# Optimization experiments

Hardware: AMD Instinct MI355X
Metric: run time of the kernel (lower is better)

Reference implementation:

```python
import jax, jax.numpy as jnp
import numpy as np

R = 10000   # relation_num
E = 256     # emb_size == hidden_size
B = 1024    # batch
L = 8       # body length (loop runs L-1 steps)


def setup_inputs() -> dict:
    key = jax.random.key(0)
    ks = jax.random.split(key, 10)
    s = 0.05
    return {
        "bodys": jax.random.randint(ks[0], (B, L), 0, R),
        "emb_w": jax.random.normal(ks[1], (R, E), jnp.float32) * s,
        "w_ih": jax.random.normal(ks[2], (4 * E, E), jnp.float32) * s,
        "w_hh": jax.random.normal(ks[3], (4 * E, E), jnp.float32) * s,
        "b_ih": jax.random.normal(ks[4], (4 * E,), jnp.float32) * s,
        "b_hh": jax.random.normal(ks[5], (4 * E,), jnp.float32) * s,
        "fc1_w": jax.random.normal(ks[6], (E, 2 * E), jnp.float32) * s,
        "fc1_b": jax.random.normal(ks[7], (E,), jnp.float32) * s,
        "fc2_w": jax.random.normal(ks[8], (R + 1, E), jnp.float32) * s,
        "fc2_b": jax.random.normal(ks[9], (R + 1,), jnp.float32) * s,
    }


def _lstm(x, w_ih, w_hh, b_ih, b_hh):
    # x: [B, L, E] -> hidden states [B, L, H] (torch gate order i,f,g,o)
    Bn, _, H = x.shape[0], x.shape[1], w_hh.shape[1]
    h0 = jnp.zeros((Bn, H), x.dtype)
    c0 = jnp.zeros((Bn, H), x.dtype)

    def step(carry, xt):
        h, c = carry
        g = xt @ w_ih.T + b_ih + h @ w_hh.T + b_hh
        i, f, gg, o = jnp.split(g, 4, axis=-1)
        c = jax.nn.sigmoid(f) * c + jax.nn.sigmoid(i) * jnp.tanh(gg)
        h = jax.nn.sigmoid(o) * jnp.tanh(c)
        return (h, c), h

    _, hs = jax.lax.scan(step, (h0, c0), x.transpose(1, 0, 2))
    return hs.transpose(1, 0, 2)


def reference(bodys, emb_w, w_ih, w_hh, b_ih, b_hh, fc1_w, fc1_b, fc2_w, fc2_b):
    x = emb_w[bodys]                       # [B, L, E] embedded body relations
    body_hid = _lstm(x, w_ih, w_hh, b_ih, b_hh)  # [B, L, E]
    Rn = emb_w.shape[0]
    prob = emb_concat = prob_sf = None
    for i in range(body_hid.shape[1] - 1):   # short fixed unroll (L-1 steps)
        if i == 0:
            emb_1 = x[:, 0, :]
            second = x[:, 1, :]
        else:
            # prob_sf @ cat(embedding(indices), body_hid[:, i])  without [B,R+1,E]
            emb_1 = prob_sf[:, :Rn] @ emb_w + prob_sf[:, Rn:] * body_hid[:, i, :]
            # relation_emb[:, i+1, :] == emb_w[i+1] broadcast over batch
            second = jnp.broadcast_to(emb_w[i + 1], emb_1.shape)
        emb_concat = jnp.concatenate([emb_1, second], axis=1)   # [B, 2E]
        prob = jax.nn.relu(emb_concat @ fc1_w.T + fc1_b) @ fc2_w.T + fc2_b  # [B, R+1]
        prob_sf = jax.nn.softmax(prob, axis=1)
    return prob, emb_concat
```

## Files before the change

### kernel.cpp

```cpp
#include <hip/hip_runtime.h>

#define Bv 1024
#define Ev 256
#define Lv 8
#define Rv 10000
#define NP1 10001
#define PS2 10240
#define NPAD 10112
#define BM 64
#define BN 128
#define NSLICE 16
#define NSLOT 158
#define RPSTRIDE 160

typedef __attribute__((ext_vector_type(8))) short bf16x8;
typedef __attribute__((ext_vector_type(4))) float f32x4;

__device__ __forceinline__ float b2f(unsigned short u) {
    union { unsigned int i; float f; } v; v.i = ((unsigned int)u) << 16; return v.f;
}
__device__ __forceinline__ unsigned short f2b(float f) {
    union { float f; unsigned int i; } v; v.f = f;
    unsigned int r = v.i + 0x7fffu + ((v.i >> 16) & 1u);
    return (unsigned short)(r >> 16);
}
__device__ __forceinline__ float ftanh(float x) {
    x = fminf(fmaxf(x, -30.f), 30.f);
    float e = __expf(2.f * x);
    return (e - 1.f) / (e + 1.f);
}
__device__ __forceinline__ void glds16(const void* g, void* l) {
    __builtin_amdgcn_global_load_lds(
        (const __attribute__((address_space(1))) void*)g,
        (__attribute__((address_space(3))) void*)l, 16, 0, 0);
}

__global__ __launch_bounds__(256) void gemm_tile(
    const unsigned short* __restrict__ A1, int lda1,
    const unsigned short* __restrict__ W1, int ldw1,
    const float* __restrict__ bias1,
    int Ktot, int kchunk, int Ncols, int mode,
    float* __restrict__ outF, unsigned short* __restrict__ outB, int ldc,
    float* __restrict__ rowPart, float* __restrict__ sfLastU)
{
    __shared__ unsigned short As[2][BM * 32];
    __shared__ unsigned short Bs[2][BN * 32];

    int bmode = mode & 7;
    int swz   = mode >> 4;
    int bx, by, bz;
    if (swz == 1) {
        int r = blockIdx.x & 7, q = blockIdx.x >> 3;
        bx = q & 15; by = r + (q >> 4) * 8; bz = 0;
        if (by >= NPAD / BN) return;
    } else if (swz == 2) {
        int r = blockIdx.x & 7, q = blockIdx.x >> 3;
        bz = r + (q >> 5) * 8; bx = (q & 31) >> 1; by = q & 1;
    } else {
        bx = blockIdx.x; by = blockIdx.y; bz = blockIdx.z;
    }

    int tid  = threadIdx.x;
    int wave = tid >> 6;
    int lane = tid & 63;
    int quad = lane >> 4;
    int l16  = lane & 15;
    int wm = (wave & 1) * 32;
    int wn = (wave >> 1) * 64;
    int m0 = bx * BM;
    int n0 = by * BN;
    int k0 = bz * kchunk;
    int k1 = k0 + kchunk; if (k1 > Ktot) k1 = Ktot;

    f32x4 acc[2][4];
#pragma unroll
    for (int i = 0; i < 2; ++i)
#pragma unroll
        for (int j = 0; j < 4; ++j) acc[i][j] = (f32x4){0.f, 0.f, 0.f, 0.f};

    int c0 = tid, c1 = 256 + tid;
    int row0 = c0 >> 2, row1 = c1 >> 2;
    int g80 = ((c0 & 3) ^ (row0 & 3) ^ ((row0 >> 2) & 3)) * 8;
    int g81 = ((c1 & 3) ^ (row1 & 3) ^ ((row1 >> 2) & 3)) * 8;

    bool first = true;
    for (int k = k0; k < k1; k += 64) {
        if (!first) __syncthreads();
        first = false;
#pragma unroll
        for (int h = 0; h < 2; ++h) {
            int kk = k + h * 32;
            glds16(A1 + (size_t)(m0 + row0) * lda1 + kk + g80, As[h] + (wave * 64) * 8);
            glds16(W1 + (size_t)(n0 + row0) * ldw1 + kk + g80, Bs[h] + (wave * 64) * 8);
            glds16(W1 + (size_t)(n0 + row1) * ldw1 + kk + g81, Bs[h] + (256 + wave * 64) * 8);
        }
        asm volatile("s_waitcnt vmcnt(0)" ::: "memory");
        __syncthreads();

#pragma unroll
        for (int h = 0; h < 2; ++h) {
            bf16x8 af[2], bfr[4];
#pragma unroll
            for (int t = 0; t < 2; ++t) {
                int m = wm + t * 16 + l16;
                int ca = quad ^ (m & 3) ^ ((m >> 2) & 3);
                af[t] = *(const bf16x8*)(As[h] + m * 32 + ca * 8);
            }
#pragma unroll
            for (int t = 0; t < 4; ++t) {
                int n = wn + t * 16 + l16;
                int cb = quad ^ (n & 3) ^ ((n >> 2) & 3);
                bfr[t] = *(const bf16x8*)(Bs[h] + n * 32 + cb * 8);
            }
#pragma unroll
            for (int i = 0; i < 2; ++i)
#pragma unroll
                for (int j = 0; j < 4; ++j)
                    acc[i][j] = __builtin_amdgcn_mfma_f32_16x16x32_bf16(
                        af[i], bfr[j], acc[i][j], 0, 0, 0);
        }
    }

    if (bmode == 5) {
        float rsum[2][4];
#pragma unroll
        for (int i = 0; i < 2; ++i)
#pragma unroll
            for (int r = 0; r < 4; ++r) rsum[i][r] = 0.f;
#pragma unroll
        for (int j = 0; j < 4; ++j) {
            int n = n0 + wn + j * 16 + l16;
            bool valid = (n < Ncols);
            float bsum = valid ? bias1[n] : 0.f;
#pragma unroll
            for (int i = 0; i < 2; ++i) {
                int mBase = m0 + wm + i * 16 + quad * 4;
#pragma unroll
                for (int r = 0; r < 4; ++r) {
                    float e = 0.f;
                    unsigned short w = 0;
                    if (valid) {
                        e = __expf(acc[i][j][r] + bsum);
                        w = f2b(e);
                        if (n == Rv) sfLastU[mBase + r] = e;
                    }
                    outB[(size_t)(mBase + r) * ldc + n] = w;
                    rsum[i][r] += e;
                }
            }
        }
        int slot = by * 2 + (wn >> 6);
#pragma unroll
        for (int i = 0; i < 2; ++i)
#pragma unroll
            for (int r = 0; r < 4; ++r) {
                float s = rsum[i][r];
                s += __shfl_xor(s, 1);
                s += __shfl_xor(s, 2);
                s += __shfl_xor(s, 4);
                s += __shfl_xor(s, 8);
                if (l16 == 0) {
                    int m = m0 + wm + i * 16 + quad * 4 + r;
                    rowPart[(size_t)m * RPSTRIDE + slot] = s;
                }
            }
        return;
    }

#pragma unroll
    for (int j = 0; j < 4; ++j) {
        int n = n0 + wn + j * 16 + l16;
        bool valid = (n < Ncols);
        if (!valid && bmode != 3) continue;
        float bsum = (valid && bias1) ? bias1[n] : 0.f;
#pragma unroll
        for (int i = 0; i < 2; ++i) {
            int mBase = m0 + wm + i * 16 + quad * 4;
#pragma unroll
            for (int r = 0; r < 4; ++r) {
                float v = acc[i][j][r] + bsum;
                size_t idx = (size_t)(mBase + r) * ldc + n;
                if (bmode == 0)      outF[idx] = v;
                else if (bmode == 3) outB[idx] = valid ? f2b(v) : (unsigned short)0;
                else                 outB[(size_t)bz * (Bv * Ev) + idx] = f2b(v);
            }
        }
    }
}

__global__ __launch_bounds__(256) void gemm64(
    const unsigned short* __restrict__ A1, int lda1,
    const unsigned short* __restrict__ W1, int ldw1,
    const float* __restrict__ bias1,
    int Ktot, int Ncols, int mode,
    float* __restrict__ outF, unsigned short* __restrict__ outB,
    int ldc, int nshift,
    const float* __restrict__ xgate, int tstep)
{
    __shared__ unsigned short As[2][64 * 32];
    __shared__ unsigned short Bs[2][64 * 32];

    int bmode = mode & 7;
    int bx = blockIdx.x >> nshift;
    int by = blockIdx.x & ((1 << nshift) - 1);
    int tid  = threadIdx.x;
    int wave = tid >> 6;
    int lane = tid & 63;
    int quad = lane >> 4;
    int l16  = lane & 15;
    int m0 = bx * 64;
    int n0 = by * 64;

    f32x4 acc[4];
#pragma unroll
    for (int j = 0; j < 4; ++j) acc[j] = (f32x4){0.f, 0.f, 0.f, 0.f};

    int row = tid >> 2;
    int g8  = ((tid & 3) ^ (row & 3) ^ ((row >> 2) & 3)) * 8;

    bool first = true;
    for (int k = 0; k < Ktot; k += 64) {
        if (!first) __syncthreads();
        first = false;
#pragma unroll
        for (int h = 0; h < 2; ++h) {
            int kk = k + h * 32;
            glds16(A1 + (size_t)(m0 + row) * lda1 + kk + g8, As[h] + wave * 512);
            glds16(W1 + (size_t)(n0 + row) * ldw1 + kk + g8, Bs[h] + wave * 512);
        }
        asm volatile("s_waitcnt vmcnt(0)" ::: "memory");
        __syncthreads();

#pragma unroll
        for (int h = 0; h < 2; ++h) {
            int ml = wave * 16 + l16;
            int ca = quad ^ (ml & 3) ^ ((ml >> 2) & 3);
            bf16x8 a = *(const bf16x8*)(As[h] + ml * 32 + ca * 8);
#pragma unroll
            for (int j = 0; j < 4; ++j) {
                int nl = j * 16 + l16;
                int cb = quad ^ (nl & 3) ^ ((nl >> 2) & 3);
                bf16x8 b = *(const bf16x8*)(Bs[h] + nl * 32 + cb * 8);
                acc[j] = __builtin_amdgcn_mfma_f32_16x16x32_bf16(a, b, acc[j], 0, 0, 0);
            }
        }
    }

    if (bmode == 4) {
        int e  = by * 16 + l16;
        float bi = bias1[n0 + l16];
        float bf_ = bias1[n0 + 16 + l16];
        float bg = bias1[n0 + 32 + l16];
        float bo = bias1[n0 + 48 + l16];
#pragma unroll
        for (int r = 0; r < 4; ++r) {
            int m = m0 + wave * 16 + quad * 4 + r;
            const float* xr = xgate + ((size_t)m * Lv + tstep) * 1024 + n0 + l16;
            float gi = acc[0][r] + bi + xr[0];
            float gf = acc[1][r] + bf_ + xr[16];
            float gg = acc[2][r] + bg + xr[32];
            float go = acc[3][r] + bo + xr[48];
            float cp = (mode & 8) ? 0.f : outF[(size_t)m * 256 + e];
            float si = 1.f / (1.f + __expf(-gi));
            float sf = 1.f / (1.f + __expf(-gf));
            float so = 1.f / (1.f + __expf(-go));
            float cn = sf * cp + si * ftanh(gg);
            outF[(size_t)m * 256 + e] = cn;
            outB[(size_t)m * 256 + e] = f2b(so * ftanh(cn));
        }
        return;
    }

#pragma unroll
    for (int j = 0; j < 4; ++j) {
        int n = n0 + j * 16 + l16;
        if (n >= Ncols) continue;
        float bsum = bias1 ? bias1[n] : 0.f;
#pragma unroll
        for (int r = 0; r < 4; ++r) {
            int m = m0 + wave * 16 + quad * 4 + r;
            float v = acc[j][r] + bsum;
            if (bmode == 1) outB[(size_t)m * ldc + n] = f2b(v > 0.f ? v : 0.f);
            else            outB[(size_t)m * ldc + n] = f2b(v);
        }
    }
}

__global__ void prep_k(const float* __restrict__ w_ih,
                       const float* __restrict__ w_hh,
                       const float* __restrict__ fc1_w,
                       const float* __restrict__ fc2_w,
                       const float* __restrict__ b_ih,
                       const float* __restrict__ b_hh,
                       const int* __restrict__ bodys,
                       const float* __restrict__ emb_w,
                       const float* __restrict__ fc1_b,
                       unsigned short* __restrict__ w_ih_b,
                       unsigned short* __restrict__ w_hh_b,
                       unsigned short* __restrict__ fc1_w_b,
                       unsigned short* __restrict__ fc2_w_b,
                       float* __restrict__ biasC,
                       unsigned short* __restrict__ x,
                       unsigned short* __restrict__ embT,
                       unsigned short* __restrict__ embc,
                       unsigned short* __restrict__ sfA,
                       float* __restrict__ B2,
                       unsigned short* __restrict__ emb_w_b,
                       unsigned short* __restrict__ EW1T)
{
    __shared__ float tile[32][33];
    int b = blockIdx.x, t = threadIdx.x;
    if (b < 1264) {
#pragma unroll
        for (int j = 0; j < 8; ++j) {
            int i = b * 2048 + j * 256 + t;
            fc2_w_b[i] = (i < NP1 * Ev) ? f2b(fc2_w[i]) : (unsigned short)0;
        }
    } else if (b < 1520) {
        int bb = b - 1264;
        const float* src = (bb < 128) ? w_ih : w_hh;
        unsigned short* dst = (bb < 128) ? w_ih_b : w_hh_b;
        int rb = (bb & 127) * 8;
#pragma unroll
        for (int j = 0; j < 8; ++j) {
            int r = rb + j;
            int gate = (r >> 4) & 3;
            int e = (r & 15) | ((r >> 6) << 4);
            dst[(size_t)r * 256 + t] = f2b(src[(size_t)(gate * 256 + e) * 256 + t]);
        }
    } else if (b < 1584) {
        int base = (b - 1520) * 2048;
#pragma unroll
        for (int j = 0; j < 8; ++j) {
            int i = base + j * 256 + t;
            fc1_w_b[i] = f2b(fc1_w[i]);
        }
    } else if (b < 1585) {
#pragma unroll
        for (int j = 0; j < 4; ++j) {
            int r = j * 256 + t;
            int gate = (r >> 4) & 3;
            int e = (r & 15) | ((r >> 6) << 4);
            biasC[r] = b_ih[gate * 256 + e] + b_hh[gate * 256 + e];
        }
    } else if (b < 2609) {
        int bb = b - 1585;
#pragma unroll
        for (int j = 0; j < 8; ++j) {
            int row = bb * 8 + j;
            x[(size_t)row * Ev + t] = f2b(emb_w[(size_t)bodys[row] * Ev + t]);
        }
    } else if (b < 5169) {
        int bb = b - 2609;
        int kt = (bb % 320) * 32, et = (bb / 320) * 32;
        int tx = t & 31, ty = t >> 5;
#pragma unroll
        for (int r = ty; r < 32; r += 8) {
            int k = kt + r;
            tile[r][tx] = (k < Rv) ? emb_w[(size_t)k * Ev + et + tx] : 0.f;
        }
        __syncthreads();
#pragma unroll
        for (int r = ty; r < 32; r += 8) {
            embT[(size_t)(et + r) * PS2 + kt + tx] = f2b(tile[tx][r]);
        }
    } else if (b < 6193) {
        int bb = b - 5169;
        embc[(size_t)bb * 512 + t]       = f2b(emb_w[(size_t)bodys[bb * Lv + 0] * Ev + t]);
        embc[(size_t)bb * 512 + 256 + t] = f2b(emb_w[(size_t)bodys[bb * Lv + 1] * Ev + t]);
        if (t < PS2 - NPAD) sfA[(size_t)bb * PS2 + NPAD + t] = 0;
    } else if (b < 6200) {
        int i = b - 6193;
        const float* er = emb_w + (size_t)(i + 1) * Ev;
        const float* wr = fc1_w + (size_t)t * 512 + 256;
        float s = fc1_b[t];
        for (int k = 0; k < 256; ++k) s += wr[k] * er[k];
        B2[i * 256 + t] = s;
    } else if (b < 7464) {
        int bb = b - 6200;
#pragma unroll
        for (int j = 0; j < 8; ++j) {
            int i = bb * 2048 + j * 256 + t;
            emb_w_b[i] = ((i >> 8) < Rv) ? f2b(emb_w[i]) : (unsigned short)0;
        }
    } else {
        int idx = (b - 7464) * 256 + t;
        EW1T[(size_t)(idx >> 7) * PS2 + NPAD + (idx & 127)] = 0;
    }
}

__global__ void finalize_emb(const unsigned short* __restrict__ emb1p,
                             const float* __restrict__ rowPart,
                             const float* __restrict__ sfLastU,
                             const unsigned short* __restrict__ h_i,
                             const float* __restrict__ emb_row,
                             unsigned short* __restrict__ embc,
                             float* __restrict__ outTail,
                             const float* __restrict__ HWrow,
                             const float* __restrict__ B2row,
                             unsigned short* __restrict__ hiddenA)
{
    int b = blockIdx.x, e = threadIdx.x;
    int wave = e >> 6, lane = e & 63;
    __shared__ float sred[4];
    float ps = (e < NSLOT) ? rowPart[(size_t)b * RPSTRIDE + e] : 0.f;
    for (int off = 32; off; off >>= 1) ps += __shfl_down(ps, off);
    if (lane == 0) sred[wave] = ps;
    __syncthreads();
    float inv = 1.f / (sred[0] + sred[1] + sred[2] + sred[3]);

    float x1 = 0.f;
#pragma unroll
    for (int z = 0; z < NSLICE; ++z)
        x1 += b2f(emb1p[(size_t)z * (Bv * Ev) + (size_t)b * Ev + e]);

    if (HWrow) {
        float v = x1 * inv + sfLastU[b] * inv * HWrow[(size_t)b * 256 + e] + B2row[e];
        hiddenA[(size_t)b * 256 + e] = f2b(v > 0.f ? v : 0.f);
    } else {
        float v = (x1 + sfLastU[b] * b2f(h_i[(size_t)b * Ev + e])) * inv;
        embc[(size_t)b * 512 + e] = f2b(v);
        float w = emb_row[e];
        embc[(size_t)b * 512 + 256 + e]    = f2b(w);
        outTail[(size_t)b * 512 + e]       = v;
        outTail[(size_t)b * 512 + 256 + e] = w;
    }
}

extern "C" void kernel_launch(void* const* d_in, const int* in_sizes, int n_in,
                              void* d_out, int out_size, void* d_ws, size_t ws_size,
                              hipStream_t stream)
{
    const int*   bodys = (const int*)d_in[0];
    const float* emb_w = (const float*)d_in[1];
    const float* w_ih  = (const float*)d_in[2];
    const float* w_hh  = (const float*)d_in[3];
    const float* b_ih  = (const float*)d_in[4];
    const float* b_hh  = (const float*)d_in[5];
    const float* fc1_w = (const float*)d_in[6];
    const float* fc1_b = (const float*)d_in[7];
    const float* fc2_w = (const float*)d_in[8];
    const float* fc2_b = (const float*)d_in[9];
    float* out = (float*)d_out;

    char* ws = (char*)d_ws;
    size_t off = 0;
    auto alloc = [&](size_t bytes) -> void* {
        void* p = ws + off;
        off += (bytes + 255) & ~(size_t)255;
        return p;
    };
    unsigned short* x       = (unsigned short*)alloc((size_t)Bv * Lv * Ev * 2);
    unsigned short* hs      = (unsigned short*)alloc((size_t)Lv * Bv * Ev * 2);
    float*          cbuf    = (float*)alloc((size_t)Bv * Ev * 4);
    float*          xg      = (float*)alloc((size_t)Bv * Lv * 1024 * 4);
    unsigned short* embT    = (unsigned short*)alloc((size_t)Ev * PS2 * 2);
    unsigned short* sfA     = (unsigned short*)alloc((size_t)Bv * PS2 * 2);
    float*          sfLastU = (float*)alloc((size_t)Bv * 4);
    float*          rowPart = (float*)alloc((size_t)Bv * RPSTRIDE * 4);
    unsigned short* emb1p   = (unsigned short*)alloc((size_t)NSLICE * Bv * Ev * 2);
    unsigned short* embc    = (unsigned short*)alloc((size_t)Bv * 512 * 2);
    unsigned short* hiddenA = (unsigned short*)alloc((size_t)Bv * Ev * 2);
    unsigned short* w_ih_b  = (unsigned short*)alloc((size_t)1024 * Ev * 2);
    unsigned short* w_hh_b  = (unsigned short*)alloc((size_t)1024 * Ev * 2);
    float*          biasC   = (float*)alloc((size_t)1024 * 4);
    float*          B2      = (float*)alloc((size_t)7 * 256 * 4);
    unsigned short* fc1_w_b = (unsigned short*)alloc((size_t)Ev * 512 * 2);
    unsigned short* fc2_w_b = (unsigned short*)alloc((size_t)NPAD * Ev * 2);
    unsigned short* emb_w_b = (unsigned short*)alloc((size_t)NPAD * Ev * 2);
    unsigned short* EW1T    = (unsigned short*)alloc((size_t)Ev * PS2 * 2);
    float*          HW      = (float*)alloc((size_t)Lv * Bv * Ev * 4);
    (void)ws_size; (void)in_sizes; (void)n_in; (void)out_size;

    prep_k<<<7592, 256, 0, stream>>>(w_ih, w_hh, fc1_w, fc2_w, b_ih, b_hh,
                                     bodys, emb_w, fc1_b,
                                     w_ih_b, w_hh_b, fc1_w_b, fc2_w_b, biasC, x,
                                     embT, embc, sfA, B2, emb_w_b, EW1T);

    gemm_tile<<<dim3(4, 79, 1), 256, 0, stream>>>(
        fc1_w_b, 512, emb_w_b, Ev,
        nullptr,
        Ev, Ev, Rv, 3,
        nullptr, EW1T, PS2, nullptr, nullptr);

    gemm64<<<64, 256, 0, stream>>>(
        embc, 512, fc1_w_b, 512,
        fc1_b,
        512, 256, 1,
        nullptr, hiddenA, 256, 2,
        nullptr, 0);

    gemm_tile<<<dim3(128, 8, 1), 256, 0, stream>>>(
        x, Ev, w_ih_b, Ev,
        nullptr,
        Ev, Ev, 1024, 0,
        xg, nullptr, 1024, nullptr, nullptr);

    for (int t = 0; t < Lv; ++t) {
        gemm64<<<256, 256, 0, stream>>>(
            hs + (size_t)(t ? t - 1 : 0) * Bv * Ev, Ev, w_hh_b, Ev,
            biasC,
            (t == 0) ? 0 : Ev, 1024, 4 | (t == 0 ? 8 : 0),
            cbuf, hs + (size_t)t * Bv * Ev, 1024, 4,
            xg, t);
    }

    gemm_tile<<<dim3(128, 2, 1), 256, 0, stream>>>(
        hs, Ev, fc1_w_b, 512,
        nullptr,
        Ev, Ev, Ev, 0,
        HW, nullptr, Ev, nullptr, nullptr);

    for (int i = 0; i < 7; ++i) {
        if (i > 0) {
            bool last = (i == 6);
            gemm_tile<<<512, 256, 0, stream>>>(
                sfA, PS2, last ? embT : EW1T, PS2,
                nullptr,
                PS2, PS2 / NSLICE, Ev, 2 | (2 << 4),
                nullptr, emb1p, Ev, nullptr, nullptr);
            finalize_emb<<<Bv, 256, 0, stream>>>(
                emb1p, rowPart, sfLastU,
                hs + (size_t)i * Bv * Ev, emb_w + (size_t)(i + 1) * Ev,
                embc, out + (size_t)Bv * NP1,
                last ? nullptr : (HW + (size_t)i * Bv * Ev),
                last ? nullptr : (B2 + (size_t)i * 256),
                hiddenA);
            if (last) {
                gemm64<<<64, 256, 0, stream>>>(
                    embc, 512, fc1_w_b, 512,
                    B2 + (size_t)6 * 256,
                    256, 256, 1,
                    nullptr, hiddenA, 256, 2,
                    nullptr, 0);
            }
        }
        if (i < 6) {
            gemm_tile<<<1280, 256, 0, stream>>>(
                hiddenA, Ev, fc2_w_b, Ev,
                fc2_b,
                Ev, Ev, NP1, 5 | (1 << 4),
                nullptr, sfA, PS2, rowPart, sfLastU);
        } else {
            gemm_tile<<<1280, 256, 0, stream>>>(
                hiddenA, Ev, fc2_w_b, Ev,
                fc2_b,
                Ev, Ev, NP1, 0 | (1 << 4),
                out, nullptr, NP1, nullptr, nullptr);
        }
    }
}
```

Before: 437.8 us.

## Fuse split-K reduction and hidden finalize into GEMM via last-block atomic counter

For the intermediate softmax-weighted embedding steps, the split-K GEMM now increments a per-tile atomic counter. The last of the 16 slice blocks for each tile sums the partials, applies the softmax normalisation and the HW/bias term, and writes the ReLU'd hidden activations. This removes a separate finalize_emb launch and its extra pass over the partials on five of the iterations. Separately, gemm64 now stages 128 K elements per loop instead of 64, which halves its barrier count at the cost of more LDS. The risk is a serialized tail, because one block per tile does the whole reduction.

```diff
diff --git a/kernel.cpp b/kernel.cpp
--- a/kernel.cpp
+++ b/kernel.cpp
@@ -41,10 +41,14 @@
     const float* __restrict__ bias1,
     int Ktot, int kchunk, int Ncols, int mode,
     float* __restrict__ outF, unsigned short* __restrict__ outB, int ldc,
-    float* __restrict__ rowPart, float* __restrict__ sfLastU)
+    float* __restrict__ rowPart, float* __restrict__ sfLastU,
+    int* __restrict__ cnt, const float* __restrict__ HWrow,
+    const float* __restrict__ B2row, unsigned short* __restrict__ hiddenA)
 {
     __shared__ unsigned short As[2][BM * 32];
     __shared__ unsigned short Bs[2][BN * 32];
+    __shared__ float rsum_s[64];
+    __shared__ int oldc;
 
     int bmode = mode & 7;
     int swz   = mode >> 4;
@@ -186,6 +190,39 @@
             }
         }
     }
+
+    if (bmode == 7) {
+        __threadfence();
+        __syncthreads();
+        if (tid == 0) oldc = atomicAdd(&cnt[bx * 2 + by], 1);
+        __syncthreads();
+        if (oldc != 15) return;
+        if (tid == 0) cnt[bx * 2 + by] = 0;
+        __threadfence();
+
+        int rloc = tid >> 2, part = tid & 3;
+        float s = 0.f;
+        for (int z = part; z < NSLOT; z += 4)
+            s += rowPart[(size_t)(m0 + rloc) * RPSTRIDE + z];
+        s += __shfl_down(s, 1);
+        s += __shfl_down(s, 2);
+        if (part == 0) rsum_s[rloc] = s;
+        __syncthreads();
+
+        for (int c = 0; c < 32; ++c) {
+            int idx = c * 256 + tid;
+            int ml = idx >> 7, el = idx & 127;
+            int mg = m0 + ml, eg = n0 + el;
+            float inv = 1.f / rsum_s[ml];
+            float x1 = 0.f;
+#pragma unroll
+            for (int z = 0; z < NSLICE; ++z)
+                x1 += b2f(outB[(size_t)z * (Bv * Ev) + (size_t)mg * 256 + eg]);
+            float v = x1 * inv + sfLastU[mg] * inv * HWrow[(size_t)mg * 256 + eg]
+                      + B2row[eg];
+            hiddenA[(size_t)mg * 256 + eg] = f2b(v > 0.f ? v : 0.f);
+        }
+    }
 }
 
 __global__ __launch_bounds__(256) void gemm64(
@@ -197,8 +234,8 @@
     int ldc, int nshift,
     const float* __restrict__ xgate, int tstep)
 {
-    __shared__ unsigned short As[2][64 * 32];
-    __shared__ unsigned short Bs[2][64 * 32];
+    __shared__ unsigned short As[4][64 * 32];
+    __shared__ unsigned short Bs[4][64 * 32];
 
     int bmode = mode & 7;
     int bx = blockIdx.x >> nshift;
@@ -219,11 +256,11 @@
     int g8  = ((tid & 3) ^ (row & 3) ^ ((row >> 2) & 3)) * 8;
 
     bool first = true;
-    for (int k = 0; k < Ktot; k += 64) {
+    for (int k = 0; k < Ktot; k += 128) {
         if (!first) __syncthreads();
         first = false;
 #pragma unroll
-        for (int h = 0; h < 2; ++h) {
+        for (int h = 0; h < 4; ++h) {
             int kk = k + h * 32;
             glds16(A1 + (size_t)(m0 + row) * lda1 + kk + g8, As[h] + wave * 512);
             glds16(W1 + (size_t)(n0 + row) * ldw1 + kk + g8, Bs[h] + wave * 512);
@@ -232,7 +269,7 @@
         __syncthreads();
 
 #pragma unroll
-        for (int h = 0; h < 2; ++h) {
+        for (int h = 0; h < 4; ++h) {
             int ml = wave * 16 + l16;
             int ca = quad ^ (ml & 3) ^ ((ml >> 2) & 3);
             bf16x8 a = *(const bf16x8*)(As[h] + ml * 32 + ca * 8);
@@ -306,7 +343,8 @@
                        unsigned short* __restrict__ sfA,
                        float* __restrict__ B2,
                        unsigned short* __restrict__ emb_w_b,
-                       unsigned short* __restrict__ EW1T)
+                       unsigned short* __restrict__ EW1T,
+                       int* __restrict__ cnt)
 {
     __shared__ float tile[32][33];
     int b = blockIdx.x, t = threadIdx.x;
@@ -369,6 +407,7 @@
         embc[(size_t)bb * 512 + t]       = f2b(emb_w[(size_t)bodys[bb * Lv + 0] * Ev + t]);
         embc[(size_t)bb * 512 + 256 + t] = f2b(emb_w[(size_t)bodys[bb * Lv + 1] * Ev + t]);
         if (t < PS2 - NPAD) sfA[(size_t)bb * PS2 + NPAD + t] = 0;
+        if (bb == 0 && t < 32) cnt[t] = 0;
     } else if (b < 6200) {
         int i = b - 6193;
         const float* er = emb_w + (size_t)(i + 1) * Ev;
@@ -395,10 +434,7 @@
                              const unsigned short* __restrict__ h_i,
                              const float* __restrict__ emb_row,
                              unsigned short* __restrict__ embc,
-                             float* __restrict__ outTail,
-                             const float* __restrict__ HWrow,
-                             const float* __restrict__ B2row,
-                             unsigned short* __restrict__ hiddenA)
+                             float* __restrict__ outTail)
 {
     int b = blockIdx.x, e = threadIdx.x;
     int wave = e >> 6, lane = e & 63;
@@ -414,17 +450,12 @@
     for (int z = 0; z < NSLICE; ++z)
         x1 += b2f(emb1p[(size_t)z * (Bv * Ev) + (size_t)b * Ev + e]);
 
-    if (HWrow) {
-        float v = x1 * inv + sfLastU[b] * inv * HWrow[(size_t)b * 256 + e] + B2row[e];
-        hiddenA[(size_t)b * 256 + e] = f2b(v > 0.f ? v : 0.f);
-    } else {
-        float v = (x1 + sfLastU[b] * b2f(h_i[(size_t)b * Ev + e])) * inv;
-        embc[(size_t)b * 512 + e] = f2b(v);
-        float w = emb_row[e];
-        embc[(size_t)b * 512 + 256 + e]    = f2b(w);
-        outTail[(size_t)b * 512 + e]       = v;
-        outTail[(size_t)b * 512 + 256 + e] = w;
-    }
+    float v = (x1 + sfLastU[b] * b2f(h_i[(size_t)b * Ev + e])) * inv;
+    embc[(size_t)b * 512 + e] = f2b(v);
+    float w = emb_row[e];
+    embc[(size_t)b * 512 + 256 + e]    = f2b(w);
+    outTail[(size_t)b * 512 + e]       = v;
+    outTail[(size_t)b * 512 + 256 + e] = w;
 }
 
 extern "C" void kernel_launch(void* const* d_in, const int* in_sizes, int n_in,
@@ -470,18 +501,20 @@
     unsigned short* emb_w_b = (unsigned short*)alloc((size_t)NPAD * Ev * 2);
     unsigned short* EW1T    = (unsigned short*)alloc((size_t)Ev * PS2 * 2);
     float*          HW      = (float*)alloc((size_t)Lv * Bv * Ev * 4);
+    int*            cnt     = (int*)alloc((size_t)32 * 4);
     (void)ws_size; (void)in_sizes; (void)n_in; (void)out_size;
 
     prep_k<<<7592, 256, 0, stream>>>(w_ih, w_hh, fc1_w, fc2_w, b_ih, b_hh,
                                      bodys, emb_w, fc1_b,
                                      w_ih_b, w_hh_b, fc1_w_b, fc2_w_b, biasC, x,
-                                     embT, embc, sfA, B2, emb_w_b, EW1T);
+                                     embT, embc, sfA, B2, emb_w_b, EW1T, cnt);
 
     gemm_tile<<<dim3(4, 79, 1), 256, 0, stream>>>(
         fc1_w_b, 512, emb_w_b, Ev,
         nullptr,
         Ev, Ev, Rv, 3,
-        nullptr, EW1T, PS2, nullptr, nullptr);
+        nullptr, EW1T, PS2, nullptr, nullptr,
+        nullptr, nullptr, nullptr, nullptr);
 
     gemm64<<<64, 256, 0, stream>>>(
         embc, 512, fc1_w_b, 512,
@@ -494,7 +527,8 @@
         x, Ev, w_ih_b, Ev,
         nullptr,
         Ev, Ev, 1024, 0,
-        xg, nullptr, 1024, nullptr, nullptr);
+        xg, nullptr, 1024, nullptr, nullptr,
+        nullptr, nullptr, nullptr, nullptr);
 
     for (int t = 0; t < Lv; ++t) {
         gemm64<<<256, 256, 0, stream>>>(
@@ -509,44 +543,49 @@
         hs, Ev, fc1_w_b, 512,
         nullptr,
         Ev, Ev, Ev, 0,
-        HW, nullptr, Ev, nullptr, nullptr);
+        HW, nullptr, Ev, nullptr, nullptr,
+        nullptr, nullptr, nullptr, nullptr);
 
     for (int i = 0; i < 7; ++i) {
-        if (i > 0) {
-            bool last = (i == 6);
+        if (i > 0 && i < 6) {
             gemm_tile<<<512, 256, 0, stream>>>(
-                sfA, PS2, last ? embT : EW1T, PS2,
+                sfA, PS2, EW1T, PS2,
+                nullptr,
+                PS2, PS2 / NSLICE, Ev, 7 | (2 << 4),
+                nullptr, emb1p, Ev, rowPart, sfLastU,
+                cnt, HW + (size_t)i * Bv * Ev, B2 + (size_t)i * 256, hiddenA);
+        } else if (i == 6) {
+            gemm_tile<<<512, 256, 0, stream>>>(
+                sfA, PS2, embT, PS2,
                 nullptr,
                 PS2, PS2 / NSLICE, Ev, 2 | (2 << 4),
-                nullptr, emb1p, Ev, nullptr, nullptr);
+                nullptr, emb1p, Ev, nullptr, nullptr,
+                nullptr, nullptr, nullptr, nullptr);
             finalize_emb<<<Bv, 256, 0, stream>>>(
                 emb1p, rowPart, sfLastU,
-                hs + (size_t)i * Bv * Ev, emb_w + (size_t)(i + 1) * Ev,
-                embc, out + (size_t)Bv * NP1,
-                last ? nullptr : (HW + (size_t)i * Bv * Ev),
-                last ? nullptr : (B2 + (size_t)i * 256),
-                hiddenA);
-            if (last) {
-                gemm64<<<64, 256, 0, stream>>>(
-                    embc, 512, fc1_w_b, 512,
-                    B2 + (size_t)6 * 256,
-                    256, 256, 1,
-                    nullptr, hiddenA, 256, 2,
-                    nullptr, 0);
-            }
+                hs + (size_t)6 * Bv * Ev, emb_w + (size_t)7 * Ev,
+                embc, out + (size_t)Bv * NP1);
+            gemm64<<<64, 256, 0, stream>>>(
+                embc, 512, fc1_w_b, 512,
+                B2 + (size_t)6 * 256,
+                256, 256, 1,
+                nullptr, hiddenA, 256, 2,
+                nullptr, 0);
         }
         if (i < 6) {
             gemm_tile<<<1280, 256, 0, stream>>>(
                 hiddenA, Ev, fc2_w_b, Ev,
                 fc2_b,
                 Ev, Ev, NP1, 5 | (1 << 4),
-                nullptr, sfA, PS2, rowPart, sfLastU);
+                nullptr, sfA, PS2, rowPart, sfLastU,
+                nullptr, nullptr, nullptr, nullptr);
         } else {
             gemm_tile<<<1280, 256, 0, stream>>>(
                 hiddenA, Ev, fc2_w_b, Ev,
                 fc2_b,
                 Ev, Ev, NP1, 0 | (1 << 4),
-                out, nullptr, NP1, nullptr, nullptr);
-        }
-    }
-}
+                out, nullptr, NP1, nullptr, nullptr,
+                nullptr, nullptr, nullptr, nullptr);
+        }
+    }
+}
```

Result: slower. 839.9 us (+91.9%).
